# Kernel optimization log

Hardware: AMD Instinct MI355X
Metric: run time of the kernel (lower is better)

## Reference

```python
import jax, jax.numpy as jnp
import numpy as np


def _unpack_int4(w_i32):
    # w_i32: [N, K//8] int32, 8 signed int4 nibbles per int32 (low nibble first)
    shifts = jnp.arange(8, dtype=jnp.int32) * 4
    nib = (w_i32[:, :, None] >> shifts[None, None, :]) & 0xF  # [N, K//8, 8]
    signed = (nib ^ 8) - 8  # map [0,15] -> [-8,7]
    N = w_i32.shape[0]
    return signed.reshape(N, -1)  # [N, K] int32 in [-8,7]


def setup_inputs() -> dict:
    key = jax.random.key(0)
    k1, k2, k3, k4, k5 = jax.random.split(key, 5)
    M, K, N, G = 4096, 4096, 14336, 128
    qx = jax.random.normal(k1, (M, K), dtype=jnp.float32)
    qxscale = jax.random.uniform(k2, (M, 1), dtype=jnp.float32, minval=0.5, maxval=1.5)
    weight_i4 = jax.random.randint(k3, (N, K // 8), 0, 2147483647, dtype=jnp.int32)
    weight_scale = jax.random.uniform(k4, (N, K // G), dtype=jnp.float32, minval=0.001, maxval=0.02)
    bias = jax.random.normal(k5, (N,), dtype=jnp.float32) * 0.02
    return {"qx": qx, "qxscale": qxscale, "weight_i4": weight_i4,
            "weight_scale": weight_scale, "bias": bias, "group_size": G}


def reference(qx, qxscale, weight_i4, weight_scale, bias, group_size):
    # 1) unpack int32 -> int4  2) per-group dequant  3) matmul  4) scale+bias  5) silu
    iweight = _unpack_int4(weight_i4)  # [N, K]
    N, K = iweight.shape
    deq_w = (iweight.astype(jnp.float32).reshape(N, K // group_size, group_size)
             * weight_scale[:, :, None]).reshape(N, K)  # [N, K]
    y = jnp.einsum('mk,nk->mn', qx, deq_w) * qxscale  # [M, N]
    y = y + bias[None, :]
    return jax.nn.silu(y)
```

## Files before the change

### kernel.cpp

```cpp
#include <hip/hip_runtime.h>
#include <hip/hip_bf16.h>
#include <stdint.h>


#define M_DIM 4096
#define K_DIM 4096
#define N_DIM 14336
#define GSZ   128

typedef __bf16 bf16x8 __attribute__((ext_vector_type(8)));
typedef __bf16 bf16x4 __attribute__((ext_vector_type(4)));
typedef float  f32x4  __attribute__((ext_vector_type(4)));

#define GLOAD16(g, l) __builtin_amdgcn_global_load_lds( \
    (const __attribute__((address_space(1))) void*)(g), \
    (__attribute__((address_space(3))) void*)(l), 16, 0, 0)

#define WAITVM(N) asm volatile("s_waitcnt vmcnt(" #N ")" ::: "memory")
#define WAITLGKM(N) asm volatile("s_waitcnt lgkmcnt(" #N ")" ::: "memory")
#define SB0() __builtin_amdgcn_sched_barrier(0)


__global__ __launch_bounds__(256) void convertA_kernel(
    const float* __restrict__ qx, __bf16* __restrict__ out)
{
    const size_t i = ((size_t)blockIdx.x * 256 + threadIdx.x) * 8;
    const float4 a = *(const float4*)(qx + i);
    const float4 b = *(const float4*)(qx + i + 4);
    bf16x8 v;
    v[0] = (__bf16)a.x; v[1] = (__bf16)a.y; v[2] = (__bf16)a.z; v[3] = (__bf16)a.w;
    v[4] = (__bf16)b.x; v[5] = (__bf16)b.y; v[6] = (__bf16)b.z; v[7] = (__bf16)b.w;
    *(bf16x8*)(out + i) = v;
}

__global__ __launch_bounds__(256) void dequantW_kernel(
    const int* __restrict__ wq, const float* __restrict__ wscale,
    __bf16* __restrict__ out)
{
    const size_t g = (size_t)blockIdx.x * 256 + threadIdx.x;
    const int n  = (int)(g >> 9);
    const int wi = (int)(g & 511);
    const float s = wscale[(size_t)n * (K_DIM / GSZ) + (wi >> 4)];
    const int w = wq[g];
    bf16x8 v;
    #pragma unroll
    for (int j = 0; j < 8; ++j) {
        const int q = ((int)((unsigned)w << (28 - 4 * j))) >> 28;
        v[j] = (__bf16)((float)q * s);
    }
    *(bf16x8*)(out + g * 8) = v;
}


constexpr int BM = 256, BN = 256, BK = 32;
constexpr int NT = K_DIM / BK;
constexpr int BUF_BYTES = 32768;

__global__ __launch_bounds__(512, 2) void gemm256_kernel(
    const __bf16* __restrict__ A,
    const __bf16* __restrict__ B,
    const float* __restrict__ qxscale,
    const float* __restrict__ bias,
    float* __restrict__ out)
{
    __shared__ __align__(16) char smem[4 * BUF_BYTES];

    const int t    = threadIdx.x;
    const int lane = t & 63;
    const int wave = t >> 6;
    const int wr   = wave >> 2;
    const int wc   = wave & 3;

    const int bid = blockIdx.x;
    const int cpx = (M_DIM / BM) * (N_DIM / BN) / 8;
    const int wg  = (bid & 7) * cpx + (bid >> 3);
    const int tiles_n = N_DIM / BN;
    const int tm = wg / tiles_n, tn = wg % tiles_n;
    const int m0 = tm * BM, n0 = tn * BN;

    const int srow = t >> 2;
    const int scb  = ((t & 3) * 16) ^ (((t >> 3) & 3) << 4);
    const char* aS = (const char*)A + (size_t)(m0 + srow) * K_DIM * 2 + scb;
    const char* bS = (const char*)B + (size_t)(n0 + srow) * K_DIM * 2 + scb;
    const size_t sweepG = (size_t)128 * K_DIM * 2;
    char* sbase = smem;

    auto STAGE_A = [&](int kt) {
        char* d = sbase + (kt & 3) * BUF_BYTES + t * 16;
        const char* s = aS + (size_t)kt * 64;
        GLOAD16(s, d);
        GLOAD16(s + sweepG, d + 8192);
    };
    auto STAGE_B = [&](int kt) {
        char* d = sbase + (kt & 3) * BUF_BYTES + 16384 + t * 16;
        const char* s = bS + (size_t)kt * 64;
        GLOAD16(s, d);
        GLOAD16(s + sweepG, d + 8192);
    };

    const int lane15 = lane & 15;
    const int pkb = ((lane >> 4) * 16) ^ (((lane >> 1) & 3) << 4);
    const int aRowB = (wr * 128 + lane15) * 64 + pkb;
    const int bRowB = (wc * 64 + lane15) * 64 + pkb + 16384;

    f32x4 acc[8][4] = {};
    bf16x8 afc[4], bfc[4];
    bf16x8 afn[4], bfn[4];
    bf16x8 af1[4];

    #define LA4(BUF, AF, BASE) do { _Pragma("unroll") \
        for (int i_ = 0; i_ < 4; ++i_) \
            AF[i_] = *(const bf16x8*)((BUF) + aRowB + ((BASE) + i_) * 1024); \
        } while (0)
    #define LB4(BUF, BF) do { _Pragma("unroll") \
        for (int n_ = 0; n_ < 4; ++n_) \
            BF[n_] = *(const bf16x8*)((BUF) + bRowB + n_ * 1024); \
        } while (0)
    #define MM16(AF, BF, AB) do { _Pragma("unroll") \
        for (int mi_ = 0; mi_ < 4; ++mi_) { _Pragma("unroll") \
            for (int ni_ = 0; ni_ < 4; ++ni_) \
                acc[(AB) + mi_][ni_] = __builtin_amdgcn_mfma_f32_16x16x32_bf16( \
                    AF[mi_], BF[ni_], acc[(AB) + mi_][ni_], 0, 0, 0); } \
        } while (0)

    STAGE_A(0); STAGE_B(0);
    STAGE_A(1); STAGE_B(1);
    STAGE_A(2); STAGE_B(2);
    WAITVM(4);
    __builtin_amdgcn_s_barrier();
    SB0();
    LA4(sbase, afc, 0);
    LB4(sbase, bfc);

    for (int it = 0; it < NT / 2; ++it) {
        {
            const int kt = 2 * it;
            const char* buf = sbase + (kt & 3) * BUF_BYTES;
            LA4(buf, af1, 4);
            if (kt + 3 < NT) { STAGE_A(kt + 3); STAGE_B(kt + 3); }
            WAITLGKM(4);
            SB0();
            __builtin_amdgcn_s_setprio(1);
            MM16(afc, bfc, 0);
            __builtin_amdgcn_s_setprio(0);
            {
                const char* nb = sbase + ((kt + 1) & 3) * BUF_BYTES;
                LA4(nb, afn, 0);
                LB4(nb, bfn);
            }
            WAITLGKM(8);
            SB0();
            __builtin_amdgcn_s_setprio(1);
            MM16(af1, bfc, 4);
            __builtin_amdgcn_s_setprio(0);
            if (kt + 3 < NT) WAITVM(4); else WAITVM(0);
            __builtin_amdgcn_s_barrier();
            SB0();
        }
        {
            const int kt = 2 * it + 1;
            const char* buf = sbase + (kt & 3) * BUF_BYTES;
            LA4(buf, af1, 4);
            if (kt + 3 < NT) { STAGE_A(kt + 3); STAGE_B(kt + 3); }
            WAITLGKM(4);
            SB0();
            __builtin_amdgcn_s_setprio(1);
            MM16(afn, bfn, 0);
            __builtin_amdgcn_s_setprio(0);
            if (kt + 1 < NT) {
                const char* nb = sbase + ((kt + 1) & 3) * BUF_BYTES;
                LA4(nb, afc, 0);
                LB4(nb, bfc);
                WAITLGKM(8);
            } else {
                WAITLGKM(0);
            }
            SB0();
            __builtin_amdgcn_s_setprio(1);
            MM16(af1, bfn, 4);
            __builtin_amdgcn_s_setprio(0);
            if (kt + 3 < NT) WAITVM(4); else WAITVM(0);
            __builtin_amdgcn_s_barrier();
            SB0();
        }
    }

    #undef LA4
    #undef LB4
    #undef MM16

    const int c_col = lane & 15;
    const int c_r4  = (lane >> 4) * 4;
    #pragma unroll
    for (int mi = 0; mi < 8; ++mi) {
        const int mg = m0 + wr * 128 + mi * 16 + c_r4;
        float qs[4];
        #pragma unroll
        for (int r = 0; r < 4; ++r) qs[r] = qxscale[mg + r];
        #pragma unroll
        for (int ni = 0; ni < 4; ++ni) {
            const int ng = n0 + wc * 64 + ni * 16 + c_col;
            const float bv = bias[ng];
            #pragma unroll
            for (int r = 0; r < 4; ++r) {
                const float y = acc[mi][ni][r] * qs[r] + bv;
                out[(size_t)(mg + r) * N_DIM + ng] = y / (1.f + __expf(-y));
            }
        }
    }
}


constexpr int FBM = 128, FBN = 128, FBK = 64;
constexpr int FLDA = 72;

__global__ __launch_bounds__(256) void gateproj_fused_kernel(
    const float* __restrict__ qx, const float* __restrict__ qxscale,
    const int* __restrict__ wq, const float* __restrict__ wscale,
    const float* __restrict__ bias, float* __restrict__ out)
{
    __shared__ __bf16 sA[FBM * FLDA];
    __shared__ __bf16 sB[FBN * FLDA];

    const int tid  = threadIdx.x;
    const int lane = tid & 63;
    const int wave = tid >> 6;
    const int wm = wave >> 1, wn = wave & 1;

    const int bid = blockIdx.x;
    const int cpx = (M_DIM / FBM) * (N_DIM / FBN) / 8;
    const int wg  = (bid & 7) * cpx + (bid >> 3);
    const int tiles_n = N_DIM / FBN;
    const int tm = wg / tiles_n, tn = wg % tiles_n;
    const int m0 = tm * FBM, n0 = tn * FBN;

    const int a_row = tid >> 4;
    const int a_col = (tid & 15) * 4;
    const float* aPtr = qx + (size_t)(m0 + a_row) * K_DIM + a_col;

    const int b_row = tid >> 1;
    const int b_wb  = (tid & 1) * 4;
    const int*   bPtr = wq     + (size_t)(n0 + b_row) * (K_DIM / 8) + b_wb;
    const float* sPtr = wscale + (size_t)(n0 + b_row) * (K_DIM / GSZ);

    float4 aReg[8];
    int    bRegW[4];
    float  bScl;
    f32x4 acc[4][4] = {};

    auto LOAD = [&](int kt) {
        const float* ap = aPtr + kt * FBK;
        #pragma unroll
        for (int i = 0; i < 8; ++i)
            aReg[i] = *(const float4*)(ap + (size_t)i * 16 * K_DIM);
        int4 b = *(const int4*)(bPtr + kt * 8);
        bRegW[0] = b.x; bRegW[1] = b.y; bRegW[2] = b.z; bRegW[3] = b.w;
        bScl = sPtr[kt >> 1];
    };

    auto STORE = [&]() {
        #pragma unroll
        for (int i = 0; i < 8; ++i) {
            bf16x4 v;
            v[0] = (__bf16)aReg[i].x; v[1] = (__bf16)aReg[i].y;
            v[2] = (__bf16)aReg[i].z; v[3] = (__bf16)aReg[i].w;
            *(bf16x4*)&sA[(a_row + i * 16) * FLDA + a_col] = v;
        }
        const int cb = (tid & 1) * 32;
        #pragma unroll
        for (int wi = 0; wi < 4; ++wi) {
            const int w = bRegW[wi];
            bf16x8 o;
            #pragma unroll
            for (int j = 0; j < 8; ++j) {
                const int v = ((int)((unsigned)w << (28 - 4 * j))) >> 28;
                o[j] = (__bf16)((float)v * bScl);
            }
            *(bf16x8*)&sB[b_row * FLDA + cb + wi * 8] = o;
        }
    };

    LOAD(0); STORE(); __syncthreads();

    const int FNT = K_DIM / FBK;
    for (int kt = 0; kt < FNT; ++kt) {
        if (kt + 1 < FNT) LOAD(kt + 1);
        #pragma unroll
        for (int kk = 0; kk < 2; ++kk) {
            bf16x8 af2[4], bfr2[4];
            const int ko = kk * 32 + (lane >> 4) * 8;
            #pragma unroll
            for (int mi = 0; mi < 4; ++mi)
                af2[mi] = *(const bf16x8*)&sA[(wm * 64 + mi * 16 + (lane & 15)) * FLDA + ko];
            #pragma unroll
            for (int ni = 0; ni < 4; ++ni)
                bfr2[ni] = *(const bf16x8*)&sB[(wn * 64 + ni * 16 + (lane & 15)) * FLDA + ko];
            #pragma unroll
            for (int mi = 0; mi < 4; ++mi)
                #pragma unroll
                for (int ni = 0; ni < 4; ++ni)
                    acc[mi][ni] = __builtin_amdgcn_mfma_f32_16x16x32_bf16(
                        af2[mi], bfr2[ni], acc[mi][ni], 0, 0, 0);
        }
        __syncthreads();
        if (kt + 1 < FNT) { STORE(); __syncthreads(); }
    }

    const int c_col = lane & 15;
    const int c_r4  = (lane >> 4) * 4;
    #pragma unroll
    for (int mi = 0; mi < 4; ++mi) {
        const int mg = m0 + wm * 64 + mi * 16 + c_r4;
        float qs[4];
        #pragma unroll
        for (int r = 0; r < 4; ++r) qs[r] = qxscale[mg + r];
        #pragma unroll
        for (int ni = 0; ni < 4; ++ni) {
            const int ng = n0 + wn * 64 + ni * 16 + c_col;
            const float bv = bias[ng];
            #pragma unroll
            for (int r = 0; r < 4; ++r) {
                const float y = acc[mi][ni][r] * qs[r] + bv;
                out[(size_t)(mg + r) * N_DIM + ng] = y / (1.f + __expf(-y));
            }
        }
    }
}


extern "C" void kernel_launch(void* const* d_in, const int* in_sizes, int n_in,
                              void* d_out, int out_size, void* d_ws, size_t ws_size,
                              hipStream_t stream) {
    const float* qx      = (const float*)d_in[0];
    const float* qxscale = (const float*)d_in[1];
    const int*   wq      = (const int*)d_in[2];
    const float* wscale  = (const float*)d_in[3];
    const float* bias    = (const float*)d_in[4];
    float* out = (float*)d_out;

    const size_t needA = (size_t)M_DIM * K_DIM * 2;
    const size_t needW = (size_t)N_DIM * K_DIM * 2;

    if (ws_size >= needA + needW) {
        __bf16* Abf = (__bf16*)d_ws;
        __bf16* Wbf = Abf + (size_t)M_DIM * K_DIM;

        hipLaunchKernelGGL(convertA_kernel, dim3(M_DIM * K_DIM / 8 / 256), dim3(256),
                           0, stream, qx, Abf);
        hipLaunchKernelGGL(dequantW_kernel, dim3(N_DIM * (K_DIM / 8) / 256), dim3(256),
                           0, stream, wq, wscale, Wbf);

        const int grid = (M_DIM / BM) * (N_DIM / BN);
        hipLaunchKernelGGL(gemm256_kernel, dim3(grid), dim3(512), 0, stream,
                           Abf, Wbf, qxscale, bias, out);
    } else {
        const int grid = (M_DIM / FBM) * (N_DIM / FBN);
        hipLaunchKernelGGL(gateproj_fused_kernel, dim3(grid), dim3(256), 0, stream,
                           qx, qxscale, wq, wscale, bias, out);
    }
}
```

Measured before the change: 510.5 us.

## Shrink GEMM tile to 128x256 with 4 waves and triple-buffered LDS

```diff
diff --git a/kernel.cpp b/kernel.cpp
--- a/kernel.cpp
+++ b/kernel.cpp
@@ -52,24 +52,22 @@
 }
 
 
-constexpr int BM = 256, BN = 256, BK = 32;
+constexpr int BM = 128, BN = 256, BK = 32;
 constexpr int NT = K_DIM / BK;
-constexpr int BUF_BYTES = 32768;
-
-__global__ __launch_bounds__(512, 2) void gemm256_kernel(
+constexpr int SLOT = 24576;
+
+__global__ __launch_bounds__(256, 2) void gemm128x256_kernel(
     const __bf16* __restrict__ A,
     const __bf16* __restrict__ B,
     const float* __restrict__ qxscale,
     const float* __restrict__ bias,
     float* __restrict__ out)
 {
-    __shared__ __align__(16) char smem[4 * BUF_BYTES];
+    __shared__ __align__(16) char smem[3 * SLOT];
 
     const int t    = threadIdx.x;
     const int lane = t & 63;
-    const int wave = t >> 6;
-    const int wr   = wave >> 2;
-    const int wc   = wave & 3;
+    const int wc   = t >> 6;
 
     const int bid = blockIdx.x;
     const int cpx = (M_DIM / BM) * (N_DIM / BN) / 8;
@@ -80,28 +78,28 @@
 
     const int srow = t >> 2;
     const int scb  = ((t & 3) * 16) ^ (((t >> 3) & 3) << 4);
-    const char* aS = (const char*)A + (size_t)(m0 + srow) * K_DIM * 2 + scb;
-    const char* bS = (const char*)B + (size_t)(n0 + srow) * K_DIM * 2 + scb;
-    const size_t sweepG = (size_t)128 * K_DIM * 2;
-    char* sbase = smem;
-
-    auto STAGE_A = [&](int kt) {
-        char* d = sbase + (kt & 3) * BUF_BYTES + t * 16;
-        const char* s = aS + (size_t)kt * 64;
-        GLOAD16(s, d);
-        GLOAD16(s + sweepG, d + 8192);
-    };
-    auto STAGE_B = [&](int kt) {
-        char* d = sbase + (kt & 3) * BUF_BYTES + 16384 + t * 16;
-        const char* s = bS + (size_t)kt * 64;
-        GLOAD16(s, d);
-        GLOAD16(s + sweepG, d + 8192);
+    const size_t KB = (size_t)K_DIM * 2;
+    const size_t sweepG = (size_t)64 * KB;
+    const char* aS = (const char*)A + (size_t)(m0 + srow) * KB + scb;
+    const char* bS = (const char*)B + (size_t)(n0 + srow) * KB + scb;
+
+    auto STAGE = [&](char* buf, int kt) {
+        const char* sa = aS + (size_t)kt * 64;
+        char* d = buf + t * 16;
+        GLOAD16(sa, d);
+        GLOAD16(sa + sweepG, d + 4096);
+        const char* sb = bS + (size_t)kt * 64;
+        char* db = buf + 8192 + t * 16;
+        GLOAD16(sb,              db);
+        GLOAD16(sb + sweepG,     db + 4096);
+        GLOAD16(sb + 2 * sweepG, db + 8192);
+        GLOAD16(sb + 3 * sweepG, db + 12288);
     };
 
     const int lane15 = lane & 15;
     const int pkb = ((lane >> 4) * 16) ^ (((lane >> 1) & 3) << 4);
-    const int aRowB = (wr * 128 + lane15) * 64 + pkb;
-    const int bRowB = (wc * 64 + lane15) * 64 + pkb + 16384;
+    const int aRowB = lane15 * 64 + pkb;
+    const int bRowB = 8192 + (wc * 64 + lane15) * 64 + pkb;
 
     f32x4 acc[8][4] = {};
     bf16x8 afc[4], bfc[4];
@@ -123,54 +121,56 @@
                     AF[mi_], BF[ni_], acc[(AB) + mi_][ni_], 0, 0, 0); } \
         } while (0)
 
-    STAGE_A(0); STAGE_B(0);
-    STAGE_A(1); STAGE_B(1);
-    STAGE_A(2); STAGE_B(2);
-    WAITVM(4);
+    char* p0 = smem;
+    char* p1 = smem + SLOT;
+    char* p2 = smem + 2 * SLOT;
+
+    STAGE(p0, 0);
+    STAGE(p1, 1);
+    WAITVM(6);
     __builtin_amdgcn_s_barrier();
     SB0();
-    LA4(sbase, afc, 0);
-    LB4(sbase, bfc);
+    LA4(p0, afc, 0);
+    LB4(p0, bfc);
 
     for (int it = 0; it < NT / 2; ++it) {
         {
             const int kt = 2 * it;
-            const char* buf = sbase + (kt & 3) * BUF_BYTES;
-            LA4(buf, af1, 4);
-            if (kt + 3 < NT) { STAGE_A(kt + 3); STAGE_B(kt + 3); }
+            if (kt + 2 < NT) STAGE(p2, kt + 2);
+            LA4(p0, af1, 4);
             WAITLGKM(4);
             SB0();
             __builtin_amdgcn_s_setprio(1);
             MM16(afc, bfc, 0);
             __builtin_amdgcn_s_setprio(0);
-            {
-                const char* nb = sbase + ((kt + 1) & 3) * BUF_BYTES;
-                LA4(nb, afn, 0);
-                LB4(nb, bfn);
-            }
+            if (kt + 2 < NT) WAITVM(6); else WAITVM(0);
+            __builtin_amdgcn_s_barrier();
+            SB0();
+            LA4(p1, afn, 0);
+            LB4(p1, bfn);
             WAITLGKM(8);
             SB0();
             __builtin_amdgcn_s_setprio(1);
             MM16(af1, bfc, 4);
             __builtin_amdgcn_s_setprio(0);
-            if (kt + 3 < NT) WAITVM(4); else WAITVM(0);
             __builtin_amdgcn_s_barrier();
             SB0();
         }
         {
             const int kt = 2 * it + 1;
-            const char* buf = sbase + (kt & 3) * BUF_BYTES;
-            LA4(buf, af1, 4);
-            if (kt + 3 < NT) { STAGE_A(kt + 3); STAGE_B(kt + 3); }
+            if (kt + 2 < NT) STAGE(p0, kt + 2);
+            LA4(p1, af1, 4);
             WAITLGKM(4);
             SB0();
             __builtin_amdgcn_s_setprio(1);
             MM16(afn, bfn, 0);
             __builtin_amdgcn_s_setprio(0);
             if (kt + 1 < NT) {
-                const char* nb = sbase + ((kt + 1) & 3) * BUF_BYTES;
-                LA4(nb, afc, 0);
-                LB4(nb, bfc);
+                if (kt + 2 < NT) WAITVM(6); else WAITVM(0);
+                __builtin_amdgcn_s_barrier();
+                SB0();
+                LA4(p2, afc, 0);
+                LB4(p2, bfc);
                 WAITLGKM(8);
             } else {
                 WAITLGKM(0);
@@ -179,10 +179,12 @@
             __builtin_amdgcn_s_setprio(1);
             MM16(af1, bfn, 4);
             __builtin_amdgcn_s_setprio(0);
-            if (kt + 3 < NT) WAITVM(4); else WAITVM(0);
-            __builtin_amdgcn_s_barrier();
-            SB0();
-        }
+            if (kt + 1 < NT) {
+                __builtin_amdgcn_s_barrier();
+                SB0();
+            }
+        }
+        char* tmp = p0; p0 = p2; p2 = p1; p1 = tmp;
     }
 
     #undef LA4
@@ -193,7 +195,7 @@
     const int c_r4  = (lane >> 4) * 4;
     #pragma unroll
     for (int mi = 0; mi < 8; ++mi) {
-        const int mg = m0 + wr * 128 + mi * 16 + c_r4;
+        const int mg = m0 + mi * 16 + c_r4;
         float qs[4];
         #pragma unroll
         for (int r = 0; r < 4; ++r) qs[r] = qxscale[mg + r];
@@ -351,7 +353,7 @@
                            0, stream, wq, wscale, Wbf);
 
         const int grid = (M_DIM / BM) * (N_DIM / BN);
-        hipLaunchKernelGGL(gemm256_kernel, dim3(grid), dim3(512), 0, stream,
+        hipLaunchKernelGGL(gemm128x256_kernel, dim3(grid), dim3(256), 0, stream,
                            Abf, Wbf, qxscale, bias, out);
     } else {
         const int grid = (M_DIM / FBM) * (N_DIM / FBN);
```

New measurement: 676.8 us. 32.6% more time.
